# Kernel tuning notes

Measured on AMD Instinct MI355X. Metric: run time of the kernel, lower is better.

The kernel has to match this reference:

```python
import jax, jax.numpy as jnp
import numpy as np

# pywt 'db2' filter bank (decomposition and reconstruction), float32
DEC_LO = jnp.array([-0.12940952255092145, 0.22414386804185735, 0.836516303737469, 0.48296291314469025], dtype=jnp.float32)
DEC_HI = jnp.array([-0.48296291314469025, 0.836516303737469, -0.22414386804185735, -0.12940952255092145], dtype=jnp.float32)
REC_LO = jnp.array([0.48296291314469025, 0.836516303737469, 0.22414386804185735, -0.12940952255092145], dtype=jnp.float32)
REC_HI = jnp.array([-0.12940952255092145, -0.22414386804185735, 0.836516303737469, -0.48296291314469025], dtype=jnp.float32)
_FLEN = 4
_DN = ('NCW', 'OIW', 'NCW')


def _convolve(x, f, stride, padding, lhs_dilation=1):
    # np.convolve-style convolution (kernel flipped) along last axis; x: (B, n)
    k = f[::-1][None, None, :]
    y = jax.lax.conv_general_dilated(x[:, None, :], k, (stride,), padding,
                                     lhs_dilation=(lhs_dilation,),
                                     dimension_numbers=_DN)
    return y[:, 0, :]


def _dwt_db2(x):
    # pywt.dwt(x, 'db2', mode='symmetric') along last axis; n even.
    # symmetric extension by flen-1=3 on each side, valid convolution, take odd indices.
    ext = jnp.concatenate([x[:, 2::-1], x, x[:, -1:-4:-1]], axis=1)[:, 1:]
    cA = _convolve(ext, DEC_LO, 2, 'VALID')  # (B, n/2+1)
    cD = _convolve(ext, DEC_HI, 2, 'VALID')
    return cA, cD


def _idwt_db2(cA, cD):
    # pywt.idwt(cA, cD, 'db2'): upsample-by-2 convolution with rec filters,
    # trimmed to length 2L - flen + 2. Equivalent to lhs_dilation=2, pad (1,1).
    lo = _convolve(cA, REC_LO, 1, [(1, 1)], lhs_dilation=2)
    hi = _convolve(cD, REC_HI, 1, [(1, 1)], lhs_dilation=2)
    return lo + hi  # (B, n)


def setup_inputs() -> dict:
    key = jax.random.key(0)
    k1, k2 = jax.random.split(key)
    B, D = 65536, 512
    x = jax.random.normal(k1, (B, D), dtype=jnp.float32)
    weight = jax.random.normal(k2, (2, D // 2 + 1), dtype=jnp.float32)
    return {"x": x, "weight": weight}


def reference(x, weight):
    shape = x.shape
    x2 = x.reshape(-1, shape[-1])
    cA, cD = _dwt_db2(x2)
    z = _idwt_db2(cA, weight[0] * cD)
    return jax.nn.leaky_relu(z.reshape(shape), negative_slope=0.01)
```

## Files before the change

### kernel.cpp

```cpp
#include <hip/hip_runtime.h>
#include <stdint.h>


#define N 512

typedef float f4v __attribute__((ext_vector_type(4)));

__global__ __launch_bounds__(256) void wavelet_kernel(
    const float* __restrict__ x,
    const float* __restrict__ w,
    float* __restrict__ out,
    int nrows)
{
    constexpr float DL0 = -0.12940952255092145f, DL1 = 0.22414386804185735f,
                    DL2 =  0.836516303737469f,   DL3 = 0.48296291314469025f;
    constexpr float DH0 = -0.48296291314469025f, DH1 = 0.836516303737469f,
                    DH2 = -0.22414386804185735f, DH3 = -0.12940952255092145f;
    constexpr float RL0 =  0.48296291314469025f, RL1 = 0.836516303737469f,
                    RL2 =  0.22414386804185735f, RL3 = -0.12940952255092145f;
    constexpr float RH0 = -0.12940952255092145f, RH1 = -0.22414386804185735f,
                    RH2 =  0.836516303737469f,   RH3 = -0.48296291314469025f;

    const int lane = threadIdx.x & 63;
    const int wid  = threadIdx.x >> 6;

    const f4v  wv = *(const f4v*)(w + 4 * lane);
    const float w4 = w[4 * lane + 4];

    const int rstep = (int)gridDim.x * 4;

    for (int row = (int)blockIdx.x * 4 + wid; row < nrows; row += rstep) {
        const size_t base = (size_t)row * N + ((size_t)lane << 3);
        f4v va = *(const f4v*)(x + base);
        f4v vb = *(const f4v*)(x + base + 4);

        float xl0 = __shfl_up(vb.z, 1);
        float xl1 = __shfl_up(vb.w, 1);
        float xr0 = __shfl_down(va.x, 1);
        float xr1 = __shfl_down(va.y, 1);
        if (lane == 0)  { xl0 = va.y; xl1 = va.x; }
        if (lane == 63) { xr0 = vb.w; xr1 = vb.z; }

        float A0 = DL3*xl0  + DL2*xl1  + DL1*va.x + DL0*va.y;
        float D0 = DH3*xl0  + DH2*xl1  + DH1*va.x + DH0*va.y;
        float A1 = DL3*va.x + DL2*va.y + DL1*va.z + DL0*va.w;
        float D1 = DH3*va.x + DH2*va.y + DH1*va.z + DH0*va.w;
        float A2 = DL3*va.z + DL2*va.w + DL1*vb.x + DL0*vb.y;
        float D2 = DH3*va.z + DH2*va.w + DH1*vb.x + DH0*vb.y;
        float A3 = DL3*vb.x + DL2*vb.y + DL1*vb.z + DL0*vb.w;
        float D3 = DH3*vb.x + DH2*vb.y + DH1*vb.z + DH0*vb.w;
        float A4 = DL3*vb.z + DL2*vb.w + DL1*xr0  + DL0*xr1;
        float D4 = DH3*vb.z + DH2*vb.w + DH1*xr0  + DH0*xr1;

        D0 *= wv.x; D1 *= wv.y; D2 *= wv.z; D3 *= wv.w; D4 *= w4;

        float z0 = RL2*A0 + RL0*A1 + RH2*D0 + RH0*D1;
        float z1 = RL3*A0 + RL1*A1 + RH3*D0 + RH1*D1;
        float z2 = RL2*A1 + RL0*A2 + RH2*D1 + RH0*D2;
        float z3 = RL3*A1 + RL1*A2 + RH3*D1 + RH1*D2;
        float z4 = RL2*A2 + RL0*A3 + RH2*D2 + RH0*D3;
        float z5 = RL3*A2 + RL1*A3 + RH3*D2 + RH1*D3;
        float z6 = RL2*A3 + RL0*A4 + RH2*D3 + RH0*D4;
        float z7 = RL3*A3 + RL1*A4 + RH3*D3 + RH1*D4;

        f4v oa, ob;
        oa.x = fmaxf(z0, 0.f) + 0.01f * fminf(z0, 0.f);
        oa.y = fmaxf(z1, 0.f) + 0.01f * fminf(z1, 0.f);
        oa.z = fmaxf(z2, 0.f) + 0.01f * fminf(z2, 0.f);
        oa.w = fmaxf(z3, 0.f) + 0.01f * fminf(z3, 0.f);
        ob.x = fmaxf(z4, 0.f) + 0.01f * fminf(z4, 0.f);
        ob.y = fmaxf(z5, 0.f) + 0.01f * fminf(z5, 0.f);
        ob.z = fmaxf(z6, 0.f) + 0.01f * fminf(z6, 0.f);
        ob.w = fmaxf(z7, 0.f) + 0.01f * fminf(z7, 0.f);

        __builtin_nontemporal_store(oa, (f4v*)(out + base));
        __builtin_nontemporal_store(ob, (f4v*)(out + base + 4));
    }
}

extern "C" void kernel_launch(void* const* d_in, const int* in_sizes, int n_in,
                              void* d_out, int out_size, void* d_ws, size_t ws_size,
                              hipStream_t stream) {
    const float* x = (const float*)d_in[0];
    const float* w = (const float*)d_in[1];
    float* out = (float*)d_out;

    const int nrows = in_sizes[0] / N;
    int blocks = (nrows + 3) / 4;
    if (blocks > 2048) blocks = 2048;
    if (blocks < 1) blocks = 1;
    wavelet_kernel<<<blocks, 256, 0, stream>>>(x, w, out, nrows);
}
```

Measured before the change: 240.2 us.

## Process eight rows per wave with all loads issued upfront, drop grid-stride loop

Each wavefront now handles a fixed block of eight consecutive rows, issuing all sixteen vector loads before computing, so more memory requests are in flight per wave. The persistent grid-stride loop capped at 2048 blocks is replaced by a grid sized to cover all rows in a single pass. This targets memory latency hiding in a bandwidth-bound kernel, at the cost of higher register pressure and many more blocks launched.

```diff
diff --git a/kernel.cpp b/kernel.cpp
--- a/kernel.cpp
+++ b/kernel.cpp
@@ -6,11 +6,11 @@
 
 typedef float f4v __attribute__((ext_vector_type(4)));
 
-__global__ __launch_bounds__(256) void wavelet_kernel(
-    const float* __restrict__ x,
-    const float* __restrict__ w,
-    float* __restrict__ out,
-    int nrows)
+__device__ __forceinline__ void row_compute(
+    const f4v va, const f4v vb,
+    const float xl0, const float xl1, const float xr0, const float xr1,
+    const f4v wv, const float w4,
+    f4v& oa, f4v& ob)
 {
     constexpr float DL0 = -0.12940952255092145f, DL1 = 0.22414386804185735f,
                     DL2 =  0.836516303737469f,   DL3 = 0.48296291314469025f;
@@ -21,60 +21,111 @@
     constexpr float RH0 = -0.12940952255092145f, RH1 = -0.22414386804185735f,
                     RH2 =  0.836516303737469f,   RH3 = -0.48296291314469025f;
 
+    float A0 = DL3*xl0  + DL2*xl1  + DL1*va.x + DL0*va.y;
+    float D0 = DH3*xl0  + DH2*xl1  + DH1*va.x + DH0*va.y;
+    float A1 = DL3*va.x + DL2*va.y + DL1*va.z + DL0*va.w;
+    float D1 = DH3*va.x + DH2*va.y + DH1*va.z + DH0*va.w;
+    float A2 = DL3*va.z + DL2*va.w + DL1*vb.x + DL0*vb.y;
+    float D2 = DH3*va.z + DH2*va.w + DH1*vb.x + DH0*vb.y;
+    float A3 = DL3*vb.x + DL2*vb.y + DL1*vb.z + DL0*vb.w;
+    float D3 = DH3*vb.x + DH2*vb.y + DH1*vb.z + DH0*vb.w;
+    float A4 = DL3*vb.z + DL2*vb.w + DL1*xr0  + DL0*xr1;
+    float D4 = DH3*vb.z + DH2*vb.w + DH1*xr0  + DH0*xr1;
+
+    D0 *= wv.x; D1 *= wv.y; D2 *= wv.z; D3 *= wv.w; D4 *= w4;
+
+    float z0 = RL2*A0 + RL0*A1 + RH2*D0 + RH0*D1;
+    float z1 = RL3*A0 + RL1*A1 + RH3*D0 + RH1*D1;
+    float z2 = RL2*A1 + RL0*A2 + RH2*D1 + RH0*D2;
+    float z3 = RL3*A1 + RL1*A2 + RH3*D1 + RH1*D2;
+    float z4 = RL2*A2 + RL0*A3 + RH2*D2 + RH0*D3;
+    float z5 = RL3*A2 + RL1*A3 + RH3*D2 + RH1*D3;
+    float z6 = RL2*A3 + RL0*A4 + RH2*D3 + RH0*D4;
+    float z7 = RL3*A3 + RL1*A4 + RH3*D3 + RH1*D4;
+
+    oa.x = fmaxf(z0, 0.f) + 0.01f * fminf(z0, 0.f);
+    oa.y = fmaxf(z1, 0.f) + 0.01f * fminf(z1, 0.f);
+    oa.z = fmaxf(z2, 0.f) + 0.01f * fminf(z2, 0.f);
+    oa.w = fmaxf(z3, 0.f) + 0.01f * fminf(z3, 0.f);
+    ob.x = fmaxf(z4, 0.f) + 0.01f * fminf(z4, 0.f);
+    ob.y = fmaxf(z5, 0.f) + 0.01f * fminf(z5, 0.f);
+    ob.z = fmaxf(z6, 0.f) + 0.01f * fminf(z6, 0.f);
+    ob.w = fmaxf(z7, 0.f) + 0.01f * fminf(z7, 0.f);
+}
+
+__device__ __forceinline__ void halo(
+    const f4v va, const f4v vb, const int lane,
+    float& xl0, float& xl1, float& xr0, float& xr1)
+{
+    xl0 = __shfl_up(vb.z, 1);
+    xl1 = __shfl_up(vb.w, 1);
+    xr0 = __shfl_down(va.x, 1);
+    xr1 = __shfl_down(va.y, 1);
+    if (lane == 0)  { xl0 = va.y; xl1 = va.x; }
+    if (lane == 63) { xr0 = vb.w; xr1 = vb.z; }
+}
+
+#define DO_ROW(VA, VB, BASE)                                            \
+    do {                                                                \
+        float xl0, xl1, xr0, xr1;                                       \
+        f4v oa, ob;                                                     \
+        halo(VA, VB, lane, xl0, xl1, xr0, xr1);                         \
+        row_compute(VA, VB, xl0, xl1, xr0, xr1, wv, w4, oa, ob);        \
+        __builtin_nontemporal_store(oa, (f4v*)(out + (BASE)));          \
+        __builtin_nontemporal_store(ob, (f4v*)(out + (BASE) + 4));      \
+    } while (0)
+
+__global__ __launch_bounds__(256) void wavelet_kernel(
+    const float* __restrict__ x,
+    const float* __restrict__ w,
+    float* __restrict__ out,
+    int nrows)
+{
     const int lane = threadIdx.x & 63;
     const int wid  = threadIdx.x >> 6;
 
     const f4v  wv = *(const f4v*)(w + 4 * lane);
     const float w4 = w[4 * lane + 4];
 
-    const int rstep = (int)gridDim.x * 4;
+    const int octet = (int)blockIdx.x * 4 + wid;
+    const int r0 = octet * 8;
+    if (r0 >= nrows) return;
 
-    for (int row = (int)blockIdx.x * 4 + wid; row < nrows; row += rstep) {
-        const size_t base = (size_t)row * N + ((size_t)lane << 3);
-        f4v va = *(const f4v*)(x + base);
-        f4v vb = *(const f4v*)(x + base + 4);
+    const size_t base0 = (size_t)r0 * N + ((size_t)lane << 3);
 
-        float xl0 = __shfl_up(vb.z, 1);
-        float xl1 = __shfl_up(vb.w, 1);
-        float xr0 = __shfl_down(va.x, 1);
-        float xr1 = __shfl_down(va.y, 1);
-        if (lane == 0)  { xl0 = va.y; xl1 = va.x; }
-        if (lane == 63) { xr0 = vb.w; xr1 = vb.z; }
+    if (r0 + 8 <= nrows) {
+        f4v va0 = *(const f4v*)(x + base0);
+        f4v vb0 = *(const f4v*)(x + base0 + 4);
+        f4v va1 = *(const f4v*)(x + base0 + 1 * N);
+        f4v vb1 = *(const f4v*)(x + base0 + 1 * N + 4);
+        f4v va2 = *(const f4v*)(x + base0 + 2 * N);
+        f4v vb2 = *(const f4v*)(x + base0 + 2 * N + 4);
+        f4v va3 = *(const f4v*)(x + base0 + 3 * N);
+        f4v vb3 = *(const f4v*)(x + base0 + 3 * N + 4);
+        f4v va4 = *(const f4v*)(x + base0 + 4 * N);
+        f4v vb4 = *(const f4v*)(x + base0 + 4 * N + 4);
+        f4v va5 = *(const f4v*)(x + base0 + 5 * N);
+        f4v vb5 = *(const f4v*)(x + base0 + 5 * N + 4);
+        f4v va6 = *(const f4v*)(x + base0 + 6 * N);
+        f4v vb6 = *(const f4v*)(x + base0 + 6 * N + 4);
+        f4v va7 = *(const f4v*)(x + base0 + 7 * N);
+        f4v vb7 = *(const f4v*)(x + base0 + 7 * N + 4);
 
-        float A0 = DL3*xl0  + DL2*xl1  + DL1*va.x + DL0*va.y;
-        float D0 = DH3*xl0  + DH2*xl1  + DH1*va.x + DH0*va.y;
-        float A1 = DL3*va.x + DL2*va.y + DL1*va.z + DL0*va.w;
-        float D1 = DH3*va.x + DH2*va.y + DH1*va.z + DH0*va.w;
-        float A2 = DL3*va.z + DL2*va.w + DL1*vb.x + DL0*vb.y;
-        float D2 = DH3*va.z + DH2*va.w + DH1*vb.x + DH0*vb.y;
-        float A3 = DL3*vb.x + DL2*vb.y + DL1*vb.z + DL0*vb.w;
-        float D3 = DH3*vb.x + DH2*vb.y + DH1*vb.z + DH0*vb.w;
-        float A4 = DL3*vb.z + DL2*vb.w + DL1*xr0  + DL0*xr1;
-        float D4 = DH3*vb.z + DH2*vb.w + DH1*xr0  + DH0*xr1;
-
-        D0 *= wv.x; D1 *= wv.y; D2 *= wv.z; D3 *= wv.w; D4 *= w4;
-
-        float z0 = RL2*A0 + RL0*A1 + RH2*D0 + RH0*D1;
-        float z1 = RL3*A0 + RL1*A1 + RH3*D0 + RH1*D1;
-        float z2 = RL2*A1 + RL0*A2 + RH2*D1 + RH0*D2;
-        float z3 = RL3*A1 + RL1*A2 + RH3*D1 + RH1*D2;
-        float z4 = RL2*A2 + RL0*A3 + RH2*D2 + RH0*D3;
-        float z5 = RL3*A2 + RL1*A3 + RH3*D2 + RH1*D3;
-        float z6 = RL2*A3 + RL0*A4 + RH2*D3 + RH0*D4;
-        float z7 = RL3*A3 + RL1*A4 + RH3*D3 + RH1*D4;
-
-        f4v oa, ob;
-        oa.x = fmaxf(z0, 0.f) + 0.01f * fminf(z0, 0.f);
-        oa.y = fmaxf(z1, 0.f) + 0.01f * fminf(z1, 0.f);
-        oa.z = fmaxf(z2, 0.f) + 0.01f * fminf(z2, 0.f);
-        oa.w = fmaxf(z3, 0.f) + 0.01f * fminf(z3, 0.f);
-        ob.x = fmaxf(z4, 0.f) + 0.01f * fminf(z4, 0.f);
-        ob.y = fmaxf(z5, 0.f) + 0.01f * fminf(z5, 0.f);
-        ob.z = fmaxf(z6, 0.f) + 0.01f * fminf(z6, 0.f);
-        ob.w = fmaxf(z7, 0.f) + 0.01f * fminf(z7, 0.f);
-
-        __builtin_nontemporal_store(oa, (f4v*)(out + base));
-        __builtin_nontemporal_store(ob, (f4v*)(out + base + 4));
+        DO_ROW(va0, vb0, base0);
+        DO_ROW(va1, vb1, base0 + 1 * N);
+        DO_ROW(va2, vb2, base0 + 2 * N);
+        DO_ROW(va3, vb3, base0 + 3 * N);
+        DO_ROW(va4, vb4, base0 + 4 * N);
+        DO_ROW(va5, vb5, base0 + 5 * N);
+        DO_ROW(va6, vb6, base0 + 6 * N);
+        DO_ROW(va7, vb7, base0 + 7 * N);
+    } else {
+        for (int r = r0; r < nrows; ++r) {
+            const size_t b = (size_t)r * N + ((size_t)lane << 3);
+            f4v va = *(const f4v*)(x + b);
+            f4v vb = *(const f4v*)(x + b + 4);
+            DO_ROW(va, vb, b);
+        }
     }
 }
 
@@ -86,8 +137,8 @@
     float* out = (float*)d_out;
 
     const int nrows = in_sizes[0] / N;
-    int blocks = (nrows + 3) / 4;
-    if (blocks > 2048) blocks = 2048;
+    const int octets = (nrows + 7) / 8;
+    int blocks = (octets + 3) / 4;
     if (blocks < 1) blocks = 1;
     wavelet_kernel<<<blocks, 256, 0, stream>>>(x, w, out, nrows);
 }
```

New measurement: 242.4 us. No clear change (+0.9%).
